# Kernel optimization log

Hardware: AMD Instinct MI355X
Metric: run time of the kernel (lower is better)

Reference implementation:

```python
import jax, jax.numpy as jnp
import numpy as np

GROUP_SIZE = 64  # quantization group size along in_features
RANK = 16
ALPHA = 1.0


def setup_inputs() -> dict:
    key = jax.random.key(0)
    ks = jax.random.split(key, 7)
    B, S, D_in, D_out = 4, 2048, 4096, 4096
    n_groups = D_in // GROUP_SIZE
    x = jax.random.normal(ks[0], (B, S, D_in), dtype=jnp.float32)
    qweight = jax.random.randint(ks[1], (D_out, D_in), 0, 16, dtype=jnp.int32)
    scales = jax.random.uniform(ks[2], (D_out, n_groups), dtype=jnp.float32) * 0.02
    zeros = jax.random.uniform(ks[3], (D_out, n_groups), dtype=jnp.float32) * 16.0
    lora_A = jax.random.normal(ks[4], (RANK, D_in), dtype=jnp.float32) / np.sqrt(D_in)
    lora_B = jax.random.normal(ks[5], (D_out, RANK), dtype=jnp.float32) * 0.01
    bias = jax.random.normal(ks[6], (D_out,), dtype=jnp.float32) * 0.02
    return {"x": x, "qweight": qweight, "scales": scales, "zeros": zeros,
            "lora_A": lora_A, "lora_B": lora_B, "bias": bias}


def _dequant(qweight, scales, zeros):
    # qweight: [O, I] int codes in [0,16); scales/zeros: [O, G] with G = I // GROUP_SIZE
    O, I = qweight.shape
    G = I // GROUP_SIZE
    q = qweight.astype(scales.dtype).reshape(O, G, GROUP_SIZE)
    w = (q - zeros[:, :, None]) * scales[:, :, None]
    return w.reshape(O, I)


def reference(x, qweight, scales, zeros, lora_A, lora_B, bias):
    # Base 4-bit dequantized matmul: y = x @ W^T
    W = _dequant(qweight, scales, zeros)            # [O, I]
    y = jnp.einsum('bsi,oi->bso', x, W)             # [B, S, O]
    # LoRA low-rank update: (alpha / rank) * (x @ A^T) @ B^T
    scaling = ALPHA / RANK
    lora = jnp.einsum('bsr,or->bso', jnp.einsum('bsi,ri->bsr', x, lora_A), lora_B)
    return y + scaling * lora + bias
```

## Files before the change

kernel.cpp:

```cpp
#include <hip/hip_runtime.h>
#include <stdint.h>
#include <stddef.h>

#define GM 8192
#define GN 4096
#define GK 4096
#define NGRP 64

typedef __bf16 bf16;
typedef __attribute__((ext_vector_type(8))) __bf16 bf16x8;
typedef __attribute__((ext_vector_type(4))) __bf16 bf16x4;
typedef __attribute__((ext_vector_type(4))) float floatx4;
typedef __attribute__((ext_vector_type(4))) int   intx4;
typedef __attribute__((ext_vector_type(8))) unsigned short ushortx8;
typedef __attribute__((ext_vector_type(4))) unsigned short ushortx4;

__device__ inline unsigned short f2bf(float f) {
  unsigned int u = __builtin_bit_cast(unsigned int, f);
  u += 0x7FFFu + ((u >> 16) & 1u);
  return (unsigned short)(u >> 16);
}
__device__ inline bf16x8 pack8(floatx4 a, floatx4 b) {
  ushortx8 u;
  u[0]=f2bf(a[0]); u[1]=f2bf(a[1]); u[2]=f2bf(a[2]); u[3]=f2bf(a[3]);
  u[4]=f2bf(b[0]); u[5]=f2bf(b[1]); u[6]=f2bf(b[2]); u[7]=f2bf(b[3]);
  return __builtin_bit_cast(bf16x8, u);
}
__device__ inline bf16x4 pack4(floatx4 a) {
  ushortx4 u;
  u[0]=f2bf(a[0]); u[1]=f2bf(a[1]); u[2]=f2bf(a[2]); u[3]=f2bf(a[3]);
  return __builtin_bit_cast(bf16x4, u);
}
__device__ inline void gll16(const void* g, void* l) {
  __builtin_amdgcn_global_load_lds(
      (const __attribute__((address_space(1))) void*)g,
      (__attribute__((address_space(3))) void*)l, 16, 0, 0);
}

__global__ __launch_bounds__(256) void qlora_prep(
    const float* __restrict__ x, bf16* __restrict__ xbf,
    const int* __restrict__ qw, const float* __restrict__ scales,
    const float* __restrict__ zeros, const float* __restrict__ lA,
    const float* __restrict__ lB, bf16* __restrict__ wbf) {
  __shared__ __align__(16) float Al[16 * 256];
  __shared__ __align__(16) float Bl[32 * 16];
  const int tid = threadIdx.x;

  if (blockIdx.x >= 2048) {
    int xb = blockIdx.x - 2048;
    #pragma unroll
    for (int t = 0; t < 4; ++t) {
      int fc = xb * 1024 + t * 256 + tid;
      int m  = fc >> 9;
      int rc = fc & 511;
      int p  = (rc & 7) ^ (m & 7);
      const float* src = x + ((size_t)fc << 3);
      floatx4 a = *(const floatx4*)src;
      floatx4 b = *(const floatx4*)(src + 4);
      *(bf16x8*)(xbf + (size_t)m * GK + ((rc >> 3) << 6) + (p << 3)) = pack8(a, b);
    }
    return;
  }

  const int n0  = (blockIdx.x & 127) * 32;
  const int kc0 = (blockIdx.x >> 7) * 256;
  #pragma unroll
  for (int t = 0; t < 4; ++t) {
    int idx = tid + t * 256;
    int r = idx >> 6, c = idx & 63;
    *(floatx4*)&Al[r * 256 + c * 4] = *(const floatx4*)&lA[(size_t)r * GK + kc0 + c * 4];
  }
  if (tid < 128) {
    int r = tid >> 2, c = tid & 3;
    *(floatx4*)&Bl[r * 16 + c * 4] = *(const floatx4*)&lB[(size_t)(n0 + r) * 16 + c * 4];
  }
  __syncthreads();

  const int klane = tid & 63;
  const int wv    = tid >> 6;
  const int k  = klane * 4;
  const int kg = kc0 + k;
  const int kb = kg & ~63;
  const int g  = kg >> 6;
  for (int it = 0; it < 8; ++it) {
    int nl = wv * 8 + it;
    int n  = n0 + nl;
    float Bv[16];
    #pragma unroll
    for (int r = 0; r < 16; ++r) Bv[r] = Bl[nl * 16 + r];
    floatx4 lacc = {0.f, 0.f, 0.f, 0.f};
    #pragma unroll
    for (int r = 0; r < 16; ++r) {
      floatx4 av = *(const floatx4*)&Al[r * 256 + k];
      lacc += av * Bv[r];
    }
    intx4 qv = *(const intx4*)&qw[(size_t)n * GK + kg];
    float s = scales[n * NGRP + g];
    float z = zeros[n * NGRP + g];
    floatx4 w;
    w[0] = ((float)qv[0] - z) * s + 0.0625f * lacc[0];
    w[1] = ((float)qv[1] - z) * s + 0.0625f * lacc[1];
    w[2] = ((float)qv[2] - z) * s + 0.0625f * lacc[2];
    w[3] = ((float)qv[3] - z) * s + 0.0625f * lacc[3];
    int p = (((kg >> 3) & 7) ^ (n & 7)) << 3;
    *(bf16x4*)&wbf[(size_t)n * GK + kb + p + (kg & 7)] = pack4(w);
  }
}

__global__ __launch_bounds__(256) void qlora_gemm_pre(
    const bf16* __restrict__ Abf, const bf16* __restrict__ Wbf,
    const float* __restrict__ bias, float* __restrict__ out) {
  __shared__ __align__(16) bf16 As[2][128 * 64];
  __shared__ __align__(16) bf16 Bs[2][128 * 64];
  const int tid  = threadIdx.x;
  const int wave = tid >> 6;
  const int lane = tid & 63;
  const int flat = blockIdx.y * gridDim.x + blockIdx.x;
  const int xcd  = flat & 7;
  const int j    = flat >> 3;
  const int m0   = (j >> 2) * 128;
  const int n0   = (xcd * 4 + (j & 3)) * 128;
  const int wm   = (wave >> 1) * 64;
  const int wn   = (wave & 1) * 64;
  const int rsw  = lane & 7;

  const char* gA = (const char*)(Abf + (size_t)(m0 + (lane >> 3)) * GK) + (lane & 7) * 16;
  const char* gB = (const char*)(Wbf + (size_t)(n0 + (lane >> 3)) * GK) + (lane & 7) * 16;

  auto stage = [&](int p, int k0) {
    #pragma unroll
    for (int i = 0; i < 4; ++i) {
      int rb = (wave * 4 + i) * 8;
      gll16(gA + (size_t)rb * (GK * 2) + k0 * 2, (char*)&As[p][0] + rb * 128);
      gll16(gB + (size_t)rb * (GK * 2) + k0 * 2, (char*)&Bs[p][0] + rb * 128);
    }
  };

  floatx4 acc[4][4] = {};
  stage(0, 0);

  for (int t = 0; t < 64; ++t) {
    const int p = t & 1;
    __syncthreads();
    if (t < 63) stage(1 - p, (t + 1) * 64);

    #pragma unroll
    for (int kk = 0; kk < 64; kk += 32) {
      const int cbase = kk >> 3;
      bf16x8 af[4], bfr[4];
      #pragma unroll
      for (int i = 0; i < 4; ++i)
        af[i] = *(const bf16x8*)&As[p][(wm + i * 16 + (lane & 15)) * 64
                                      + (((cbase + (lane >> 4)) ^ rsw) << 3)];
      #pragma unroll
      for (int i = 0; i < 4; ++i)
        bfr[i] = *(const bf16x8*)&Bs[p][(wn + i * 16 + (lane & 15)) * 64
                                        + (((cbase + (lane >> 4)) ^ rsw) << 3)];
      #pragma unroll
      for (int mi = 0; mi < 4; ++mi)
        #pragma unroll
        for (int ni = 0; ni < 4; ++ni)
          acc[mi][ni] = __builtin_amdgcn_mfma_f32_16x16x32_bf16(af[mi], bfr[ni], acc[mi][ni], 0, 0, 0);
    }
  }

  const int quad = lane >> 4;
  const int col  = lane & 15;
  #pragma unroll
  for (int ni = 0; ni < 4; ++ni) {
    int gn = n0 + wn + ni * 16 + col;
    float bv = bias[gn];
    #pragma unroll
    for (int mi = 0; mi < 4; ++mi) {
      int gm = m0 + wm + mi * 16 + quad * 4;
      #pragma unroll
      for (int r = 0; r < 4; ++r)
        out[(size_t)(gm + r) * GN + gn] = acc[mi][ni][r] + bv;
    }
  }
}

__global__ void qlora_gemm_fb(const float* __restrict__ x, const int* __restrict__ qw,
                              const float* __restrict__ scales, const float* __restrict__ zeros,
                              const float* __restrict__ bias, float* __restrict__ out) {
  __shared__ __align__(16) bf16 As[128 * 64];
  __shared__ __align__(16) bf16 Bs[128 * 64];
  const int tid  = threadIdx.x;
  const int wave = tid >> 6;
  const int lane = tid & 63;
  const int m0 = blockIdx.x * 128;
  const int n0 = blockIdx.y * 128;
  const int wm = (wave >> 1) * 64;
  const int wn = (wave & 1) * 64;
  const int rsw = lane & 7;
  floatx4 acc[4][4] = {};
  for (int k0 = 0; k0 < GK; k0 += 64) {
    int row = tid >> 1, kh = (tid & 1) * 32;
    {
      const float* gx = x + (size_t)(m0 + row) * GK + k0 + kh;
      #pragma unroll
      for (int jj = 0; jj < 4; ++jj) {
        floatx4 a = *(const floatx4*)(gx + jj * 8);
        floatx4 b = *(const floatx4*)(gx + jj * 8 + 4);
        int p = (((kh >> 3) + jj) ^ (row & 7)) << 3;
        *(bf16x8*)&As[row * 64 + p] = pack8(a, b);
      }
    }
    {
      int n = n0 + row;
      int g = k0 >> 6;
      float s = scales[n * NGRP + g];
      float z = zeros[n * NGRP + g];
      const int* gq = qw + (size_t)n * GK + k0 + kh;
      #pragma unroll
      for (int jj = 0; jj < 4; ++jj) {
        intx4 q0 = *(const intx4*)(gq + jj * 8);
        intx4 q1 = *(const intx4*)(gq + jj * 8 + 4);
        floatx4 a, b;
        a[0]=((float)q0[0]-z)*s; a[1]=((float)q0[1]-z)*s; a[2]=((float)q0[2]-z)*s; a[3]=((float)q0[3]-z)*s;
        b[0]=((float)q1[0]-z)*s; b[1]=((float)q1[1]-z)*s; b[2]=((float)q1[2]-z)*s; b[3]=((float)q1[3]-z)*s;
        int p = (((kh >> 3) + jj) ^ (row & 7)) << 3;
        *(bf16x8*)&Bs[row * 64 + p] = pack8(a, b);
      }
    }
    __syncthreads();
    #pragma unroll
    for (int kk = 0; kk < 64; kk += 32) {
      const int cbase = kk >> 3;
      bf16x8 af[4], bfr[4];
      #pragma unroll
      for (int i = 0; i < 4; ++i)
        af[i] = *(const bf16x8*)&As[(wm + i * 16 + (lane & 15)) * 64
                                    + (((cbase + (lane >> 4)) ^ rsw) << 3)];
      #pragma unroll
      for (int i = 0; i < 4; ++i)
        bfr[i] = *(const bf16x8*)&Bs[(wn + i * 16 + (lane & 15)) * 64
                                     + (((cbase + (lane >> 4)) ^ rsw) << 3)];
      #pragma unroll
      for (int mi = 0; mi < 4; ++mi)
        #pragma unroll
        for (int ni = 0; ni < 4; ++ni)
          acc[mi][ni] = __builtin_amdgcn_mfma_f32_16x16x32_bf16(af[mi], bfr[ni], acc[mi][ni], 0, 0, 0);
    }
    __syncthreads();
  }
  const int quad = lane >> 4;
  const int col  = lane & 15;
  #pragma unroll
  for (int ni = 0; ni < 4; ++ni) {
    int gn = n0 + wn + ni * 16 + col;
    float bv = bias[gn];
    #pragma unroll
    for (int mi = 0; mi < 4; ++mi) {
      int gm = m0 + wm + mi * 16 + quad * 4;
      #pragma unroll
      for (int r = 0; r < 4; ++r)
        out[(size_t)(gm + r) * GN + gn] = acc[mi][ni][r] + bv;
    }
  }
}

extern "C" void kernel_launch(void* const* d_in, const int* in_sizes, int n_in,
                              void* d_out, int out_size, void* d_ws, size_t ws_size,
                              hipStream_t stream) {
  (void)in_sizes; (void)n_in; (void)out_size;
  const float* x      = (const float*)d_in[0];
  const int*   qw     = (const int*)d_in[1];
  const float* scales = (const float*)d_in[2];
  const float* zeros  = (const float*)d_in[3];
  const float* lA     = (const float*)d_in[4];
  const float* lB     = (const float*)d_in[5];
  const float* bias   = (const float*)d_in[6];
  float* out = (float*)d_out;

  const size_t xbf_bytes = (size_t)GM * GK * sizeof(bf16);
  const size_t wbf_bytes = (size_t)GN * GK * sizeof(bf16);
  char* ws = (char*)d_ws;

  if (ws_size >= xbf_bytes + wbf_bytes) {
    bf16* xbf = (bf16*)ws;
    bf16* wbf = (bf16*)(ws + xbf_bytes);
    qlora_prep<<<dim3(2048 + 4096), 256, 0, stream>>>(x, xbf, qw, scales, zeros, lA, lB, wbf);
    qlora_gemm_pre<<<dim3(GM / 128, GN / 128), 256, 0, stream>>>(xbf, wbf, bias, out);
  } else {
    qlora_gemm_fb<<<dim3(GM / 128, GN / 128), 256, 0, stream>>>(x, qw, scales, zeros, bias, out);
  }
}
```

Measured before the change: 592.6 us.

## Use 256x256 tiles with 8 waves and phased LDS/MFMA pipelining

Switches the bf16 GEMM from 128x128 tiles with 4 waves to 256x256 tiles with 8 waves. The K loop is split into four phases that interleave half-tile global-to-LDS loads, LDS fragment reads and MFMA bursts, using explicit barriers, vmcnt waits and s_setprio. The aim is more data reuse per tile and better overlap of memory traffic with matrix math. In exchange it needs 128 KB of LDS per block and many accumulator registers, and the hand-written wait counts could cause race hazards if they are wrong.

```diff
diff --git a/kernel.cpp b/kernel.cpp
--- a/kernel.cpp
+++ b/kernel.cpp
@@ -107,77 +107,145 @@
   }
 }
 
-__global__ __launch_bounds__(256) void qlora_gemm_pre(
+__global__ __launch_bounds__(512, 2) void qlora_gemm_pre(
     const bf16* __restrict__ Abf, const bf16* __restrict__ Wbf,
     const float* __restrict__ bias, float* __restrict__ out) {
-  __shared__ __align__(16) bf16 As[2][128 * 64];
-  __shared__ __align__(16) bf16 Bs[2][128 * 64];
+  __shared__ __align__(16) bf16 As[2][256 * 64];
+  __shared__ __align__(16) bf16 Bs[2][256 * 64];
   const int tid  = threadIdx.x;
   const int wave = tid >> 6;
   const int lane = tid & 63;
-  const int flat = blockIdx.y * gridDim.x + blockIdx.x;
+  const int wr   = wave >> 2;
+  const int wc   = wave & 3;
+
+  const int flat = blockIdx.x;
   const int xcd  = flat & 7;
   const int j    = flat >> 3;
-  const int m0   = (j >> 2) * 128;
-  const int n0   = (xcd * 4 + (j & 3)) * 128;
-  const int wm   = (wave >> 1) * 64;
-  const int wn   = (wave & 1) * 64;
-  const int rsw  = lane & 7;
-
-  const char* gA = (const char*)(Abf + (size_t)(m0 + (lane >> 3)) * GK) + (lane & 7) * 16;
-  const char* gB = (const char*)(Wbf + (size_t)(n0 + (lane >> 3)) * GK) + (lane & 7) * 16;
-
-  auto stage = [&](int p, int k0) {
-    #pragma unroll
-    for (int i = 0; i < 4; ++i) {
-      int rb = (wave * 4 + i) * 8;
-      gll16(gA + (size_t)rb * (GK * 2) + k0 * 2, (char*)&As[p][0] + rb * 128);
-      gll16(gB + (size_t)rb * (GK * 2) + k0 * 2, (char*)&Bs[p][0] + rb * 128);
+  const int m0   = (j >> 1) * 256;
+  const int n0   = (xcd * 2 + (j & 1)) * 256;
+
+  const int srow = tid >> 3;
+  const int schk = tid & 7;
+  const bf16* gA = Abf + (size_t)(m0 + srow) * GK + schk * 8;
+  const bf16* gB = Wbf + (size_t)(n0 + srow) * GK + schk * 8;
+  char* lA = (char*)&As[0][0] + srow * 128 + schk * 16;
+  char* lB = (char*)&Bs[0][0] + srow * 128 + schk * 16;
+
+  auto stageA = [&](int buf, int tk, int half) {
+    #pragma unroll
+    for (int r = 0; r < 2; ++r) {
+      int rb = half * 128 + r * 64;
+      gll16(gA + (size_t)rb * GK + tk * 64, lA + buf * 32768 + rb * 128);
     }
   };
-
-  floatx4 acc[4][4] = {};
-  stage(0, 0);
+  auto stageB = [&](int buf, int tk, int half) {
+    #pragma unroll
+    for (int r = 0; r < 2; ++r) {
+      int rb = half * 128 + r * 64;
+      gll16(gB + (size_t)rb * GK + tk * 64, lB + buf * 32768 + rb * 128);
+    }
+  };
+
+  const int rs   = lane & 7;
+  const int hi   = lane >> 4;
+  const int rofs = (lane & 15) * 64;
+  const int c0   = ((0 + hi) ^ rs) << 3;
+  const int c1   = ((4 + hi) ^ rs) << 3;
+  const int arow = wr * 64;
+  const int brow = wc * 32;
+
+  bf16x8 af[4][2];
+  bf16x8 bv[2][2];
+  floatx4 acc[8][4] = {};
+
+#define DSLOAD_A(P, MH) { \
+    const bf16* Ap_ = &As[P][(MH * 128 + arow) * 64 + rofs]; \
+    _Pragma("unroll") \
+    for (int mi = 0; mi < 4; ++mi) { \
+      af[mi][0] = *(const bf16x8*)(Ap_ + mi * 16 * 64 + c0); \
+      af[mi][1] = *(const bf16x8*)(Ap_ + mi * 16 * 64 + c1); \
+    } }
+#define DSLOAD_B(P, NH) { \
+    const bf16* Bp_ = &Bs[P][(NH * 128 + brow) * 64 + rofs]; \
+    _Pragma("unroll") \
+    for (int ni = 0; ni < 2; ++ni) { \
+      bv[ni][0] = *(const bf16x8*)(Bp_ + ni * 16 * 64 + c0); \
+      bv[ni][1] = *(const bf16x8*)(Bp_ + ni * 16 * 64 + c1); \
+    } }
+#define MFMA_PH(MH, NH) { \
+    _Pragma("unroll") \
+    for (int kk = 0; kk < 2; ++kk) \
+      _Pragma("unroll") \
+      for (int mi = 0; mi < 4; ++mi) \
+        _Pragma("unroll") \
+        for (int ni = 0; ni < 2; ++ni) \
+          acc[MH * 4 + mi][NH * 2 + ni] = __builtin_amdgcn_mfma_f32_16x16x32_bf16( \
+              af[mi][kk], bv[ni][kk], acc[MH * 4 + mi][NH * 2 + ni], 0, 0, 0); \
+  }
+#define BAR() __builtin_amdgcn_s_barrier()
+#define LGKM0() asm volatile("s_waitcnt lgkmcnt(0)" ::: "memory")
+#define PRIO(N) __builtin_amdgcn_s_setprio(N)
+
+  stageA(0, 0, 0); stageA(0, 0, 1); stageB(0, 0, 0); stageB(0, 0, 1);
+  stageA(1, 1, 0); stageB(1, 1, 1); stageA(1, 1, 1);
+  asm volatile("s_waitcnt vmcnt(6)" ::: "memory");
+  BAR();
 
   for (int t = 0; t < 64; ++t) {
     const int p = t & 1;
-    __syncthreads();
-    if (t < 63) stage(1 - p, (t + 1) * 64);
-
-    #pragma unroll
-    for (int kk = 0; kk < 64; kk += 32) {
-      const int cbase = kk >> 3;
-      bf16x8 af[4], bfr[4];
-      #pragma unroll
-      for (int i = 0; i < 4; ++i)
-        af[i] = *(const bf16x8*)&As[p][(wm + i * 16 + (lane & 15)) * 64
-                                      + (((cbase + (lane >> 4)) ^ rsw) << 3)];
-      #pragma unroll
-      for (int i = 0; i < 4; ++i)
-        bfr[i] = *(const bf16x8*)&Bs[p][(wn + i * 16 + (lane & 15)) * 64
-                                        + (((cbase + (lane >> 4)) ^ rsw) << 3)];
-      #pragma unroll
-      for (int mi = 0; mi < 4; ++mi)
-        #pragma unroll
-        for (int ni = 0; ni < 4; ++ni)
-          acc[mi][ni] = __builtin_amdgcn_mfma_f32_16x16x32_bf16(af[mi], bfr[ni], acc[mi][ni], 0, 0, 0);
-    }
-  }
+    DSLOAD_A(p, 0); DSLOAD_B(p, 0);
+    if (t < 63) stageB(1 - p, t + 1, 0);
+    BAR(); LGKM0();
+    PRIO(1); MFMA_PH(0, 0); PRIO(0);
+    BAR();
+    DSLOAD_B(p, 1);
+    if (t < 62) stageA(p, t + 2, 0);
+    BAR(); LGKM0();
+    PRIO(1); MFMA_PH(0, 1); PRIO(0);
+    BAR();
+    DSLOAD_A(p, 1);
+    if (t < 62) stageB(p, t + 2, 1);
+    BAR(); LGKM0();
+    PRIO(1); MFMA_PH(1, 1); PRIO(0);
+    BAR();
+    DSLOAD_B(p, 0);
+    if (t < 62) {
+      stageA(p, t + 2, 1);
+      asm volatile("s_waitcnt vmcnt(6)" ::: "memory");
+    } else {
+      asm volatile("s_waitcnt vmcnt(0)" ::: "memory");
+    }
+    BAR(); LGKM0();
+    PRIO(1); MFMA_PH(1, 0); PRIO(0);
+    BAR();
+  }
+
+#undef DSLOAD_A
+#undef DSLOAD_B
+#undef MFMA_PH
+#undef BAR
+#undef LGKM0
+#undef PRIO
 
   const int quad = lane >> 4;
   const int col  = lane & 15;
   #pragma unroll
-  for (int ni = 0; ni < 4; ++ni) {
-    int gn = n0 + wn + ni * 16 + col;
-    float bv = bias[gn];
-    #pragma unroll
-    for (int mi = 0; mi < 4; ++mi) {
-      int gm = m0 + wm + mi * 16 + quad * 4;
-      #pragma unroll
-      for (int r = 0; r < 4; ++r)
-        out[(size_t)(gm + r) * GN + gn] = acc[mi][ni][r] + bv;
-    }
-  }
+  for (int nh = 0; nh < 2; ++nh)
+    #pragma unroll
+    for (int ni = 0; ni < 2; ++ni) {
+      const int gn = n0 + nh * 128 + wc * 32 + ni * 16 + col;
+      const float bvv = bias[gn];
+      #pragma unroll
+      for (int mh = 0; mh < 2; ++mh)
+        #pragma unroll
+        for (int mi = 0; mi < 4; ++mi) {
+          const int gm = m0 + mh * 128 + wr * 64 + mi * 16 + quad * 4;
+          floatx4 a = acc[mh * 4 + mi][nh * 2 + ni];
+          #pragma unroll
+          for (int r = 0; r < 4; ++r)
+            out[(size_t)(gm + r) * GN + gn] = a[r] + bvv;
+        }
+    }
 }
 
 __global__ void qlora_gemm_fb(const float* __restrict__ x, const int* __restrict__ qw,
@@ -281,7 +349,7 @@
     bf16* xbf = (bf16*)ws;
     bf16* wbf = (bf16*)(ws + xbf_bytes);
     qlora_prep<<<dim3(2048 + 4096), 256, 0, stream>>>(x, xbf, qw, scales, zeros, lA, lB, wbf);
-    qlora_gemm_pre<<<dim3(GM / 128, GN / 128), 256, 0, stream>>>(xbf, wbf, bias, out);
+    qlora_gemm_pre<<<dim3((GM / 256) * (GN / 256)), 512, 0, stream>>>(xbf, wbf, bias, out);
   } else {
     qlora_gemm_fb<<<dim3(GM / 128, GN / 128), 256, 0, stream>>>(x, qw, scales, zeros, bias, out);
   }
```

Measured after the change: 536.5 us. 1.1x faster.
